# Performance work log

Measured on AMD Instinct MI355X. Metric: run time of the kernel, lower is better.

## Reference

```python
import jax, jax.numpy as jnp
import numpy as np

N_NODES = 50000
N_EDGES = 800000
LN_EPS = 1e-5


def setup_inputs() -> dict:
    key = jax.random.key(0)
    ks = jax.random.split(key, 6)
    B, N, D = 2, N_NODES, 128
    x = jax.random.normal(ks[0], (B, N, D), dtype=jnp.float32)
    A_rows = jax.random.randint(ks[1], (N_EDGES,), 0, N, dtype=jnp.int32)
    A_cols = jax.random.randint(ks[2], (N_EDGES,), 0, N, dtype=jnp.int32)
    A_vals = jax.random.uniform(ks[3], (N_EDGES,), dtype=jnp.float32)
    W = jax.random.normal(ks[4], (D, D), dtype=jnp.float32) * (1.0 / np.sqrt(D))
    b = jnp.zeros((D,), dtype=jnp.float32)
    gamma = jnp.ones((D,), dtype=jnp.float32)
    beta = jnp.zeros((D,), dtype=jnp.float32)
    return {"x": x, "A_rows": A_rows, "A_cols": A_cols, "A_vals": A_vals,
            "W": W, "b": b, "gamma": gamma, "beta": beta}


def reference(x, A_rows, A_cols, A_vals, W, b, gamma, beta):
    B, N, D = x.shape
    # SpMM: A @ x2 where x2 = x.transpose(0,1).reshape(N, B*D)
    x2 = jnp.transpose(x, (1, 0, 2)).reshape(N, B * D)  # [N, B*D]
    msgs = x2[A_cols] * A_vals[:, None]                 # [E, B*D]
    y2 = jax.ops.segment_sum(msgs, A_rows, num_segments=N)  # [N, B*D]
    out = jnp.transpose(y2.reshape(N, B, D), (1, 0, 2))  # [B, N, D]
    # Linear -> LayerNorm -> GELU (dropout = identity in eval)
    h = out @ W + b
    mu = jnp.mean(h, axis=-1, keepdims=True)
    var = jnp.var(h, axis=-1, keepdims=True)
    h = (h - mu) * jax.lax.rsqrt(var + LN_EPS) * gamma + beta
    return jax.nn.gelu(h, approximate=False)
```

## Files before the change

kernel.cpp:

```cpp
#include <hip/hip_runtime.h>
#include <hip/hip_fp16.h>
#include <cstdint>
#include <cstddef>

#define N_NODES 50000
#define N_EDGES 800000
#define D 128
#define M_ROWS (2 * N_NODES)
#define N_TILES (M_ROWS / 16)
#define TILES_PER_BATCH (N_NODES / 16)
#define CAP 64
#define LN_EPS 1e-5f

typedef __attribute__((ext_vector_type(8))) short bf16x8;
typedef __attribute__((ext_vector_type(4))) float f32x4;

__device__ inline unsigned short bf16_rne(float f) {
  unsigned u = __float_as_uint(f);
  unsigned r = (u + 0x7FFFu + ((u >> 16) & 1u)) >> 16;
  return (unsigned short)r;
}

__global__ __launch_bounds__(256) void k_scatter_prep(
    const float* __restrict__ W,
    unsigned short* __restrict__ wt_hi,
    unsigned short* __restrict__ wt_lo,
    const int* __restrict__ rows,
    const int* __restrict__ cols,
    const float* __restrict__ vals,
    int* __restrict__ cnt,
    int2* __restrict__ epair) {
  int b = blockIdx.x;
  if (b < 64) {
    int i = b * 256 + threadIdx.x;
    int d = i >> 7, j = i & 127;
    float v = W[i];
    unsigned short hb = bf16_rne(v);
    float rem = v - __uint_as_float((unsigned)hb << 16);
    wt_hi[j * 128 + d] = hb;
    wt_lo[j * 128 + d] = bf16_rne(rem);
    return;
  }
  int base = (b - 64) * 1024 + threadIdx.x * 4;
  if (base + 3 < N_EDGES) {
    int4 rr = *reinterpret_cast<const int4*>(&rows[base]);
    int4 cc = *reinterpret_cast<const int4*>(&cols[base]);
    float4 vv = *reinterpret_cast<const float4*>(&vals[base]);
    int p0 = atomicAdd(&cnt[rr.x], 1);
    int p1 = atomicAdd(&cnt[rr.y], 1);
    int p2 = atomicAdd(&cnt[rr.z], 1);
    int p3 = atomicAdd(&cnt[rr.w], 1);
    if (p0 < CAP) epair[rr.x * CAP + p0] = int2{cc.x, __float_as_int(vv.x)};
    if (p1 < CAP) epair[rr.y * CAP + p1] = int2{cc.y, __float_as_int(vv.y)};
    if (p2 < CAP) epair[rr.z * CAP + p2] = int2{cc.z, __float_as_int(vv.z)};
    if (p3 < CAP) epair[rr.w * CAP + p3] = int2{cc.w, __float_as_int(vv.w)};
  } else {
    for (int e = base; e < N_EDGES; e++) {
      int r = rows[e];
      int pos = atomicAdd(&cnt[r], 1);
      if (pos < CAP) epair[r * CAP + pos] = int2{cols[e], __float_as_int(vals[e])};
    }
  }
}

__global__ __launch_bounds__(512) void k_gemm_z(const float* __restrict__ x,
                                                const unsigned short* __restrict__ wt_hi,
                                                const unsigned short* __restrict__ wt_lo,
                                                __half* __restrict__ z) {
  __shared__ unsigned short lw[2][128 * 128];
  int tid = threadIdx.x;

  for (int c = tid; c < 2048; c += 512) {
    int j = c >> 4;
    int k16 = c & 15;
    int soff = j * 256 + ((k16 * 16) ^ ((j & 7) << 4));
    *reinterpret_cast<float4*>(reinterpret_cast<char*>(lw[0]) + soff) =
        *reinterpret_cast<const float4*>(wt_hi + j * 128 + k16 * 8);
    *reinterpret_cast<float4*>(reinterpret_cast<char*>(lw[1]) + soff) =
        *reinterpret_cast<const float4*>(wt_lo + j * 128 + k16 * 8);
  }

  int wave = tid >> 6, l = tid & 63;
  int tile = blockIdx.x * 8 + wave;
  bool active = tile < N_TILES;
  int lrow = l & 15;
  int kg = l >> 4;

  float4 xv[4][2];
  if (active) {
    const float* xr = x + (size_t)(tile * 16 + lrow) * D + kg * 8;
#pragma unroll
    for (int kc = 0; kc < 4; kc++) {
      xv[kc][0] = *reinterpret_cast<const float4*>(xr + kc * 32);
      xv[kc][1] = *reinterpret_cast<const float4*>(xr + kc * 32 + 4);
    }
  } else {
#pragma unroll
    for (int kc = 0; kc < 4; kc++) {
      xv[kc][0] = float4{0.f, 0.f, 0.f, 0.f};
      xv[kc][1] = float4{0.f, 0.f, 0.f, 0.f};
    }
  }
  __syncthreads();

  bf16x8 ahi[4], alo[4];
#pragma unroll
  for (int kc = 0; kc < 4; kc++) {
    float tmp[8];
    *reinterpret_cast<float4*>(&tmp[0]) = xv[kc][0];
    *reinterpret_cast<float4*>(&tmp[4]) = xv[kc][1];
    bf16x8 h, lo8;
#pragma unroll
    for (int e = 0; e < 8; e++) {
      unsigned short hb = bf16_rne(tmp[e]);
      float rem = tmp[e] - __uint_as_float((unsigned)hb << 16);
      h[e] = (short)hb;
      lo8[e] = (short)bf16_rne(rem);
    }
    ahi[kc] = h; alo[kc] = lo8;
  }

  f32x4 acc[8];
#pragma unroll
  for (int jt = 0; jt < 8; jt++) acc[jt] = (f32x4){0.f, 0.f, 0.f, 0.f};

#pragma unroll
  for (int kc = 0; kc < 4; kc++) {
#pragma unroll
    for (int jt = 0; jt < 8; jt++) {
      int j = jt * 16 + lrow;
      int kbyte = kc * 64 + kg * 16;
      int soff = j * 256 + (kbyte ^ ((j & 7) << 4));
      bf16x8 bhi = *reinterpret_cast<bf16x8*>(reinterpret_cast<char*>(lw[0]) + soff);
      bf16x8 blo = *reinterpret_cast<bf16x8*>(reinterpret_cast<char*>(lw[1]) + soff);
      acc[jt] = __builtin_amdgcn_mfma_f32_16x16x32_bf16(ahi[kc], bhi, acc[jt], 0, 0, 0);
      acc[jt] = __builtin_amdgcn_mfma_f32_16x16x32_bf16(alo[kc], bhi, acc[jt], 0, 0, 0);
      acc[jt] = __builtin_amdgcn_mfma_f32_16x16x32_bf16(ahi[kc], blo, acc[jt], 0, 0, 0);
    }
  }

  __syncthreads();
  unsigned short* lds = &lw[0][0] + (size_t)wave * 2176;
  int rbase = kg * 4;
#pragma unroll
  for (int jt = 0; jt < 8; jt++) {
#pragma unroll
    for (int r = 0; r < 4; r++) {
      __half hv = __float2half(acc[jt][r]);
      lds[(rbase + r) * 136 + jt * 16 + lrow] = __half_as_ushort(hv);
    }
  }
  __syncthreads();
  if (active) {
    int bb = (tile >= TILES_PER_BATCH);
    int n0 = tile * 16 - bb * N_NODES;
    const char* ldsb = reinterpret_cast<const char*>(lds);
    char* zb = reinterpret_cast<char*>(z);
#pragma unroll
    for (int r = 0; r < 16; r++) {
      unsigned v = *reinterpret_cast<const unsigned*>(ldsb + r * 272 + 4 * l);
      *reinterpret_cast<unsigned*>(zb + (size_t)(n0 + r) * 512 + bb * 256 + 4 * l) = v;
    }
  }
}

__device__ inline float gelu_exact(float v) {
  return 0.5f * v * (1.0f + erff(v * 0.70710678118654752440f));
}

__global__ __launch_bounds__(256) void k_spmm_ln(const __half* __restrict__ z,
                                                 const int* __restrict__ cnt,
                                                 const int2* __restrict__ epair,
                                                 const float* __restrict__ bias,
                                                 const float* __restrict__ gamma,
                                                 const float* __restrict__ beta,
                                                 float* __restrict__ out) {
  int unit = blockIdx.x * 4 + (threadIdx.x >> 6);
  int l = threadIdx.x & 63;
  int node = unit >> 1;
  int plane = unit & 1;

  int end = cnt[node];
  if (end > CAP) end = CAP;
  const int2* ep = epair + (size_t)node * CAP;

  const char* zc = reinterpret_cast<const char*>(z) + plane * 256 + 4 * l;
  float2 acc = {0.f, 0.f};

  int k = 0;
  for (; k + 3 < end; k += 4) {
    int2 e0 = ep[k];
    int2 e1 = ep[k + 1];
    int2 e2 = ep[k + 2];
    int2 e3 = ep[k + 3];
    unsigned p0 = *reinterpret_cast<const unsigned*>(zc + (size_t)e0.x * 512);
    unsigned p1 = *reinterpret_cast<const unsigned*>(zc + (size_t)e1.x * 512);
    unsigned p2 = *reinterpret_cast<const unsigned*>(zc + (size_t)e2.x * 512);
    unsigned p3 = *reinterpret_cast<const unsigned*>(zc + (size_t)e3.x * 512);
    float v0 = __int_as_float(e0.y), v1 = __int_as_float(e1.y);
    float v2 = __int_as_float(e2.y), v3 = __int_as_float(e3.y);
    float2 f0 = __half22float2(*reinterpret_cast<const __half2*>(&p0));
    float2 f1 = __half22float2(*reinterpret_cast<const __half2*>(&p1));
    float2 f2 = __half22float2(*reinterpret_cast<const __half2*>(&p2));
    float2 f3 = __half22float2(*reinterpret_cast<const __half2*>(&p3));
    acc.x += v0 * f0.x; acc.y += v0 * f0.y;
    acc.x += v1 * f1.x; acc.y += v1 * f1.y;
    acc.x += v2 * f2.x; acc.y += v2 * f2.y;
    acc.x += v3 * f3.x; acc.y += v3 * f3.y;
  }
  for (; k < end; k++) {
    int2 e0 = ep[k];
    unsigned p0 = *reinterpret_cast<const unsigned*>(zc + (size_t)e0.x * 512);
    float v0 = __int_as_float(e0.y);
    float2 f0 = __half22float2(*reinterpret_cast<const __half2*>(&p0));
    acc.x += v0 * f0.x; acc.y += v0 * f0.y;
  }

  int j0 = 2 * l;
  float2 bv = *reinterpret_cast<const float2*>(&bias[j0]);
  float2 gv = *reinterpret_cast<const float2*>(&gamma[j0]);
  float2 ev = *reinterpret_cast<const float2*>(&beta[j0]);

  float h0 = acc.x + bv.x, h1 = acc.y + bv.y;
  float s = h0 + h1;
  float q = h0 * h0 + h1 * h1;
#pragma unroll
  for (int o = 32; o >= 1; o >>= 1) {
    s += __shfl_xor(s, o, 64);
    q += __shfl_xor(q, o, 64);
  }
  float mu = s * (1.0f / 128.0f);
  float var = q * (1.0f / 128.0f) - mu * mu;
  float inv = rsqrtf(var + LN_EPS);

  float2 o2;
  o2.x = gelu_exact((h0 - mu) * inv * gv.x + ev.x);
  o2.y = gelu_exact((h1 - mu) * inv * gv.y + ev.y);

  *reinterpret_cast<float2*>(
      &out[(size_t)plane * N_NODES * D + (size_t)node * D + j0]) = o2;
}

extern "C" void kernel_launch(void* const* d_in, const int* in_sizes, int n_in,
                              void* d_out, int out_size, void* d_ws, size_t ws_size,
                              hipStream_t stream) {
  const float* x      = (const float*)d_in[0];
  const int*   A_rows = (const int*)d_in[1];
  const int*   A_cols = (const int*)d_in[2];
  const float* A_vals = (const float*)d_in[3];
  const float* W      = (const float*)d_in[4];
  const float* b      = (const float*)d_in[5];
  const float* gamma  = (const float*)d_in[6];
  const float* beta   = (const float*)d_in[7];
  float* out = (float*)d_out;

  char* ws = (char*)d_ws;
  size_t off = 0;
  auto alloc = [&](size_t bytes) {
    char* p = ws + off;
    off += (bytes + 255) & ~(size_t)255;
    return p;
  };
  __half*         zbuf  = (__half*)alloc((size_t)M_ROWS * D * sizeof(__half));
  int*            cnt   = (int*)alloc((size_t)N_NODES * sizeof(int));
  int2*           epair = (int2*)alloc((size_t)N_NODES * CAP * sizeof(int2));
  unsigned short* wt_hi = (unsigned short*)alloc(128 * 128 * sizeof(unsigned short));
  unsigned short* wt_lo = (unsigned short*)alloc(128 * 128 * sizeof(unsigned short));

  hipMemsetAsync(cnt, 0, N_NODES * sizeof(int), stream);

  k_scatter_prep<<<64 + (N_EDGES / 4 + 255) / 256, 256, 0, stream>>>(
      W, wt_hi, wt_lo, A_rows, A_cols, A_vals, cnt, epair);
  k_gemm_z<<<(N_TILES + 7) / 8, 512, 0, stream>>>(x, wt_hi, wt_lo, zbuf);
  k_spmm_ln<<<(2 * N_NODES) / 4, 256, 0, stream>>>(zbuf, cnt, epair, b, gamma,
                                                   beta, out);
}
```

Measured before the change: 257.8 us.

## Process both batch planes per wavefront in SpMM+LayerNorm with wider gathers

Each wavefront now handles one node across both batch planes, with lanes 0-31 covering plane 0 and lanes 32-63 covering plane 1. Each lane gathers 8 bytes (four halves) per edge, so the edge list and its index/value pairs are read once per node instead of once per plane. An 8-way unrolled loop issues more gathers before any are consumed. The LayerNorm reduction shrinks to 32-lane groups and stores become float4. This halves the number of waves, which lowers occupancy, and uses more registers per lane.

```diff
diff --git a/kernel.cpp b/kernel.cpp
--- a/kernel.cpp
+++ b/kernel.cpp
@@ -175,57 +175,68 @@
                                                  const float* __restrict__ gamma,
                                                  const float* __restrict__ beta,
                                                  float* __restrict__ out) {
-  int unit = blockIdx.x * 4 + (threadIdx.x >> 6);
+  int r = blockIdx.x * 4 + (threadIdx.x >> 6);
   int l = threadIdx.x & 63;
-  int node = unit >> 1;
-  int plane = unit & 1;
-
-  int end = cnt[node];
+  int end = cnt[r];
   if (end > CAP) end = CAP;
-  const int2* ep = epair + (size_t)node * CAP;
-
-  const char* zc = reinterpret_cast<const char*>(z) + plane * 256 + 4 * l;
-  float2 acc = {0.f, 0.f};
+  const int2* ep = epair + (size_t)r * CAP;
+
+  const char* zc = reinterpret_cast<const char*>(z) + 8 * l;
+  float4 acc = {0.f, 0.f, 0.f, 0.f};
 
   int k = 0;
+  for (; k + 7 < end; k += 8) {
+    int2 e[8];
+    uint2 p[8];
+#pragma unroll
+    for (int u = 0; u < 8; u++) e[u] = ep[k + u];
+#pragma unroll
+    for (int u = 0; u < 8; u++)
+      p[u] = *reinterpret_cast<const uint2*>(zc + (size_t)e[u].x * 512);
+#pragma unroll
+    for (int u = 0; u < 8; u++) {
+      float v = __int_as_float(e[u].y);
+      float2 lo = __half22float2(*reinterpret_cast<const __half2*>(&p[u].x));
+      float2 hi = __half22float2(*reinterpret_cast<const __half2*>(&p[u].y));
+      acc.x += v * lo.x; acc.y += v * lo.y; acc.z += v * hi.x; acc.w += v * hi.y;
+    }
+  }
   for (; k + 3 < end; k += 4) {
-    int2 e0 = ep[k];
-    int2 e1 = ep[k + 1];
-    int2 e2 = ep[k + 2];
-    int2 e3 = ep[k + 3];
-    unsigned p0 = *reinterpret_cast<const unsigned*>(zc + (size_t)e0.x * 512);
-    unsigned p1 = *reinterpret_cast<const unsigned*>(zc + (size_t)e1.x * 512);
-    unsigned p2 = *reinterpret_cast<const unsigned*>(zc + (size_t)e2.x * 512);
-    unsigned p3 = *reinterpret_cast<const unsigned*>(zc + (size_t)e3.x * 512);
-    float v0 = __int_as_float(e0.y), v1 = __int_as_float(e1.y);
-    float v2 = __int_as_float(e2.y), v3 = __int_as_float(e3.y);
-    float2 f0 = __half22float2(*reinterpret_cast<const __half2*>(&p0));
-    float2 f1 = __half22float2(*reinterpret_cast<const __half2*>(&p1));
-    float2 f2 = __half22float2(*reinterpret_cast<const __half2*>(&p2));
-    float2 f3 = __half22float2(*reinterpret_cast<const __half2*>(&p3));
-    acc.x += v0 * f0.x; acc.y += v0 * f0.y;
-    acc.x += v1 * f1.x; acc.y += v1 * f1.y;
-    acc.x += v2 * f2.x; acc.y += v2 * f2.y;
-    acc.x += v3 * f3.x; acc.y += v3 * f3.y;
+    int2 e[4];
+    uint2 p[4];
+#pragma unroll
+    for (int u = 0; u < 4; u++) e[u] = ep[k + u];
+#pragma unroll
+    for (int u = 0; u < 4; u++)
+      p[u] = *reinterpret_cast<const uint2*>(zc + (size_t)e[u].x * 512);
+#pragma unroll
+    for (int u = 0; u < 4; u++) {
+      float v = __int_as_float(e[u].y);
+      float2 lo = __half22float2(*reinterpret_cast<const __half2*>(&p[u].x));
+      float2 hi = __half22float2(*reinterpret_cast<const __half2*>(&p[u].y));
+      acc.x += v * lo.x; acc.y += v * lo.y; acc.z += v * hi.x; acc.w += v * hi.y;
+    }
   }
   for (; k < end; k++) {
     int2 e0 = ep[k];
-    unsigned p0 = *reinterpret_cast<const unsigned*>(zc + (size_t)e0.x * 512);
+    uint2 p0 = *reinterpret_cast<const uint2*>(zc + (size_t)e0.x * 512);
     float v0 = __int_as_float(e0.y);
-    float2 f0 = __half22float2(*reinterpret_cast<const __half2*>(&p0));
-    acc.x += v0 * f0.x; acc.y += v0 * f0.y;
-  }
-
-  int j0 = 2 * l;
-  float2 bv = *reinterpret_cast<const float2*>(&bias[j0]);
-  float2 gv = *reinterpret_cast<const float2*>(&gamma[j0]);
-  float2 ev = *reinterpret_cast<const float2*>(&beta[j0]);
-
-  float h0 = acc.x + bv.x, h1 = acc.y + bv.y;
-  float s = h0 + h1;
-  float q = h0 * h0 + h1 * h1;
-#pragma unroll
-  for (int o = 32; o >= 1; o >>= 1) {
+    float2 lo = __half22float2(*reinterpret_cast<const __half2*>(&p0.x));
+    float2 hi = __half22float2(*reinterpret_cast<const __half2*>(&p0.y));
+    acc.x += v0 * lo.x; acc.y += v0 * lo.y; acc.z += v0 * hi.x; acc.w += v0 * hi.y;
+  }
+
+  int p = l >> 5;
+  int j0 = (l & 31) * 4;
+  float4 bv = *reinterpret_cast<const float4*>(&bias[j0]);
+  float4 gv = *reinterpret_cast<const float4*>(&gamma[j0]);
+  float4 ev = *reinterpret_cast<const float4*>(&beta[j0]);
+
+  float h0 = acc.x + bv.x, h1 = acc.y + bv.y, h2 = acc.z + bv.z, h3 = acc.w + bv.w;
+  float s = h0 + h1 + h2 + h3;
+  float q = h0 * h0 + h1 * h1 + h2 * h2 + h3 * h3;
+#pragma unroll
+  for (int o = 16; o >= 1; o >>= 1) {
     s += __shfl_xor(s, o, 64);
     q += __shfl_xor(q, o, 64);
   }
@@ -233,12 +244,13 @@
   float var = q * (1.0f / 128.0f) - mu * mu;
   float inv = rsqrtf(var + LN_EPS);
 
-  float2 o2;
-  o2.x = gelu_exact((h0 - mu) * inv * gv.x + ev.x);
-  o2.y = gelu_exact((h1 - mu) * inv * gv.y + ev.y);
-
-  *reinterpret_cast<float2*>(
-      &out[(size_t)plane * N_NODES * D + (size_t)node * D + j0]) = o2;
+  float4 o4;
+  o4.x = gelu_exact((h0 - mu) * inv * gv.x + ev.x);
+  o4.y = gelu_exact((h1 - mu) * inv * gv.y + ev.y);
+  o4.z = gelu_exact((h2 - mu) * inv * gv.z + ev.z);
+  o4.w = gelu_exact((h3 - mu) * inv * gv.w + ev.w);
+
+  *reinterpret_cast<float4*>(&out[(size_t)p * N_NODES * D + (size_t)r * D + j0]) = o4;
 }
 
 extern "C" void kernel_launch(void* const* d_in, const int* in_sizes, int n_in,
@@ -272,6 +284,5 @@
   k_scatter_prep<<<64 + (N_EDGES / 4 + 255) / 256, 256, 0, stream>>>(
       W, wt_hi, wt_lo, A_rows, A_cols, A_vals, cnt, epair);
   k_gemm_z<<<(N_TILES + 7) / 8, 512, 0, stream>>>(x, wt_hi, wt_lo, zbuf);
-  k_spmm_ln<<<(2 * N_NODES) / 4, 256, 0, stream>>>(zbuf, cnt, epair, b, gamma,
-                                                   beta, out);
-}
+  k_spmm_ln<<<N_NODES / 4, 256, 0, stream>>>(zbuf, cnt, epair, b, gamma, beta, out);
+}
```

Result: faster. 234.7 us (-9.0%).
